# Optimization experiments

Measured on AMD Instinct MI355X. Metric: run time of the kernel, lower is better.

The kernel has to match this reference:

```python
import jax, jax.numpy as jnp
import numpy as np

N = 100000
B = 1024
NODE_DIM = 128
LATENT = 128
IN_DIM = NODE_DIM + 2 * LATENT   # 384, q/kv projection input width
FFN_IN = LATENT + IN_DIM          # 512, ffn input width


def setup_inputs() -> dict:
    key = jax.random.key(0)
    ks = jax.random.split(key, 16)
    s = 1.0 / np.sqrt(IN_DIM)
    s2 = 1.0 / np.sqrt(FFN_IN)
    s3 = 1.0 / np.sqrt(LATENT)
    return {
        "x": jax.random.normal(ks[0], (N, NODE_DIM), jnp.float32),
        "memory": jax.random.normal(ks[1], (N, LATENT), jnp.float32),
        "delta_t_vec": jax.random.normal(ks[2], (N, LATENT), jnp.float32),
        "tar_t_vec": jax.random.normal(ks[3], (B, LATENT), jnp.float32),
        # sparse neighbor mask, ~50 neighbors per target on average
        "neighbor_mask": jax.random.uniform(ks[4], (B, N)) < 5e-4,
        "tar_idx": jax.random.randint(ks[5], (B, 1), 0, N, jnp.int32),
        "Wq": jax.random.uniform(ks[6], (LATENT, IN_DIM), jnp.float32, -s, s),
        "bq": jnp.zeros((LATENT,), jnp.float32),
        "Wk": jax.random.uniform(ks[7], (LATENT, IN_DIM), jnp.float32, -s, s),
        "bk": jnp.zeros((LATENT,), jnp.float32),
        "Wv": jax.random.uniform(ks[8], (LATENT, IN_DIM), jnp.float32, -s, s),
        "bv": jnp.zeros((LATENT,), jnp.float32),
        "W1": jax.random.uniform(ks[9], (LATENT, FFN_IN), jnp.float32, -s2, s2),
        "b1": jnp.zeros((LATENT,), jnp.float32),
        "W2": jax.random.uniform(ks[10], (LATENT, LATENT), jnp.float32, -s3, s3),
        "b2": jnp.zeros((LATENT,), jnp.float32),
    }


def reference(x, memory, delta_t_vec, tar_t_vec, neighbor_mask, tar_idx,
              Wq, bq, Wk, bk, Wv, bv, W1, b1, W2, b2):
    idx = tar_idx[:, 0]                                  # [B]
    q_input = jnp.concatenate([x[idx], memory[idx], tar_t_vec], axis=-1)   # [B, IN_DIM]
    kv_input = jnp.concatenate([x, memory, delta_t_vec], axis=-1)          # [N, IN_DIM]
    q = q_input @ Wq.T + bq                              # [B, D]
    k = kv_input @ Wk.T + bk                             # [N, D]
    v = kv_input @ Wv.T + bv                             # [N, D]
    d = q.shape[-1]
    scores = jnp.einsum("bd,nd->bn", q, k) / jnp.sqrt(jnp.float32(d))      # [B, N]
    # rows with no neighbors attend to their own target node
    no_neighbor = ~jnp.any(neighbor_mask, axis=1)        # [B]
    self_mask = jnp.arange(neighbor_mask.shape[1])[None, :] == tar_idx     # [B, N]
    mask = neighbor_mask | (no_neighbor[:, None] & self_mask)
    scores = jnp.where(mask, scores, -jnp.inf)
    attn = jax.nn.softmax(scores, axis=-1)               # [B, N]
    agg = attn @ v                                       # [B, D]
    z = jnp.concatenate([agg, q_input], axis=-1)         # [B, FFN_IN]
    z = jax.nn.relu(z @ W1.T + b1) @ W2.T + b2           # [B, D]
    return z
```

## Files before the change

### kernel.cpp

```cpp
#include <hip/hip_runtime.h>
#include <stdint.h>
#include <stddef.h>

constexpr int N_NODES = 100000;
constexpr int BATCH   = 1024;
constexpr int LAT     = 128;
constexpr int INDIM   = 384;
constexpr int FFNIN   = 512;
constexpr int NB_MAX  = 512;

__global__ __launch_bounds__(384) void fused_graph_attn_kernel(
    const float* __restrict__ x,   const float* __restrict__ mem,
    const float* __restrict__ dtv, const float* __restrict__ ttv,
    const uint32_t* __restrict__ mask, const int* __restrict__ tar_idx,
    const float* __restrict__ Wq, const float* __restrict__ bq,
    const float* __restrict__ Wk, const float* __restrict__ bk,
    const float* __restrict__ Wv, const float* __restrict__ bv,
    const float* __restrict__ W1, const float* __restrict__ b1,
    const float* __restrict__ W2, const float* __restrict__ b2,
    float* __restrict__ out)
{
    const int b    = blockIdx.x;
    const int tid  = threadIdx.x;
    const int lane = tid & 63;
    const int wave = tid >> 6;

    __shared__ int   cnt;
    __shared__ int   jl[NB_MAX];
    __shared__ float sc[NB_MAX];
    __shared__ float qin[INDIM];
    __shared__ float qv[LAT];
    __shared__ float qk[INDIM];
    __shared__ float u[INDIM];
    __shared__ float zbuf[FFNIN];
    __shared__ float hbuf[LAT];
    __shared__ float sbias_sh;

    const int idx = tar_idx[b];
    if (tid == 0) cnt = 0;

    if (tid < 128)      qin[tid] = x[(size_t)idx * LAT + tid];
    else if (tid < 256) qin[tid] = mem[(size_t)idx * LAT + (tid - 128)];
    else                qin[tid] = ttv[(size_t)b * LAT + (tid - 256)];
    __syncthreads();

    {
        const uint4* row = (const uint4*)(mask + (size_t)b * N_NODES);
        for (int i = tid; i < N_NODES / 4; i += 384) {
            uint4 v = row[i];
            if (v.x | v.y | v.z | v.w) {
                uint32_t w[4] = {v.x, v.y, v.z, v.w};
                #pragma unroll
                for (int wi = 0; wi < 4; ++wi) {
                    if (w[wi]) {
                        int slot = atomicAdd(&cnt, 1);
                        if (slot < NB_MAX) jl[slot] = i * 4 + wi;
                    }
                }
            }
        }
    }
    __syncthreads();
    if (tid == 0 && cnt == 0) { jl[0] = idx; cnt = 1; }
    __syncthreads();
    const int nb = cnt < NB_MAX ? cnt : NB_MAX;

    if (tid < LAT) {
        const float4* wr = (const float4*)(Wq + (size_t)tid * INDIM);
        float acc = bq[tid];
        #pragma unroll 4
        for (int i = 0; i < INDIM / 4; ++i) {
            float4 w = wr[i];
            acc += w.x * qin[4*i] + w.y * qin[4*i+1] + w.z * qin[4*i+2] + w.w * qin[4*i+3];
        }
        qv[tid] = acc;
    }
    __syncthreads();

    {
        float acc = 0.f;
        #pragma unroll 8
        for (int d = 0; d < LAT; ++d) acc += qv[d] * Wk[(size_t)d * INDIM + tid];
        qk[tid] = acc;
    }
    if (wave == 0) {
        float p = qv[lane] * bk[lane] + qv[lane + 64] * bk[lane + 64];
        for (int off = 32; off; off >>= 1) p += __shfl_down(p, off, 64);
        if (lane == 0) sbias_sh = p;
    }
    __syncthreads();

    const float scale = 0.088388347648318447f;
    const float sb = sbias_sh;
    for (int jj = wave; jj < nb; jj += 6) {
        int j = jl[jj];
        const float* xp = x   + (size_t)j * LAT;
        const float* mp = mem + (size_t)j * LAT;
        const float* dp = dtv + (size_t)j * LAT;
        float p = qk[lane]       * xp[lane] + qk[lane + 64]  * xp[lane + 64]
                + qk[128 + lane] * mp[lane] + qk[192 + lane] * mp[lane + 64]
                + qk[256 + lane] * dp[lane] + qk[320 + lane] * dp[lane + 64];
        for (int off = 32; off; off >>= 1) p += __shfl_down(p, off, 64);
        if (lane == 0) sc[jj] = (p + sb) * scale;
    }
    __syncthreads();

    if (wave == 0) {
        float m = -INFINITY;
        for (int t = lane; t < nb; t += 64) m = fmaxf(m, sc[t]);
        for (int off = 32; off; off >>= 1) m = fmaxf(m, __shfl_down(m, off, 64));
        m = __shfl(m, 0, 64);
        float s = 0.f;
        for (int t = lane; t < nb; t += 64) { float e = __expf(sc[t] - m); sc[t] = e; s += e; }
        for (int off = 32; off; off >>= 1) s += __shfl_down(s, off, 64);
        s = __shfl(s, 0, 64);
        float inv = 1.f / s;
        for (int t = lane; t < nb; t += 64) sc[t] *= inv;
    }
    __syncthreads();

    {
        const float* src = (tid < 128) ? x : (tid < 256 ? mem : dtv);
        const int off128 = tid & 127;
        float acc = 0.f;
        for (int jj = 0; jj < nb; ++jj)
            acc += sc[jj] * src[(size_t)jl[jj] * LAT + off128];
        u[tid] = acc;
    }
    __syncthreads();

    if (tid < LAT) {
        const float4* wr = (const float4*)(Wv + (size_t)tid * INDIM);
        float acc = bv[tid];
        #pragma unroll 4
        for (int i = 0; i < INDIM / 4; ++i) {
            float4 w = wr[i];
            acc += w.x * u[4*i] + w.y * u[4*i+1] + w.z * u[4*i+2] + w.w * u[4*i+3];
        }
        zbuf[tid] = acc;
    }
    zbuf[LAT + tid] = qin[tid];
    __syncthreads();

    if (tid < LAT) {
        const float4* wr = (const float4*)(W1 + (size_t)tid * FFNIN);
        float acc = b1[tid];
        #pragma unroll 4
        for (int i = 0; i < FFNIN / 4; ++i) {
            float4 w = wr[i];
            acc += w.x * zbuf[4*i] + w.y * zbuf[4*i+1] + w.z * zbuf[4*i+2] + w.w * zbuf[4*i+3];
        }
        hbuf[tid] = fmaxf(acc, 0.f);
    }
    __syncthreads();

    if (tid < LAT) {
        const float4* wr = (const float4*)(W2 + (size_t)tid * LAT);
        float acc = b2[tid];
        #pragma unroll 4
        for (int i = 0; i < LAT / 4; ++i) {
            float4 w = wr[i];
            acc += w.x * hbuf[4*i] + w.y * hbuf[4*i+1] + w.z * hbuf[4*i+2] + w.w * hbuf[4*i+3];
        }
        out[(size_t)b * LAT + tid] = acc;
    }
}

extern "C" void kernel_launch(void* const* d_in, const int* in_sizes, int n_in,
                              void* d_out, int out_size, void* d_ws, size_t ws_size,
                              hipStream_t stream) {
    const float*    x    = (const float*)d_in[0];
    const float*    mem  = (const float*)d_in[1];
    const float*    dtv  = (const float*)d_in[2];
    const float*    ttv  = (const float*)d_in[3];
    const uint32_t* mask = (const uint32_t*)d_in[4];
    const int*      tidx = (const int*)d_in[5];
    const float*    Wq   = (const float*)d_in[6];
    const float*    bq   = (const float*)d_in[7];
    const float*    Wk   = (const float*)d_in[8];
    const float*    bk   = (const float*)d_in[9];
    const float*    Wv   = (const float*)d_in[10];
    const float*    bv   = (const float*)d_in[11];
    const float*    W1   = (const float*)d_in[12];
    const float*    b1   = (const float*)d_in[13];
    const float*    W2   = (const float*)d_in[14];
    const float*    b2   = (const float*)d_in[15];
    float* out = (float*)d_out;

    fused_graph_attn_kernel<<<BATCH, 384, 0, stream>>>(
        x, mem, dtv, ttv, mask, tidx, Wq, bq, Wk, bk, Wv, bv, W1, b1, W2, b2,
        out);
}
```

Before: 713.8 us.

## Overlap q projection with mask scan, fuse online softmax into aggregation

Wave 0 computes the q projection, the bias term and the qk = q·Wk vector while the other five waves scan the mask row using nontemporal loads. The score, softmax and weighted-sum phases are fused into one per-wave online-softmax pass, which removes the second gather of neighbor rows and two barriers. The per-wave partials are merged through shared memory. The final Wv, W1 and W2 matvecs are split across all 384 threads in three K-slices with a shared reduction. The catch is that only five waves scan the mask, and wave 0 does the serialized q/qk work alone.

```diff
diff --git a/kernel.cpp b/kernel.cpp
--- a/kernel.cpp
+++ b/kernel.cpp
@@ -8,6 +8,12 @@
 constexpr int INDIM   = 384;
 constexpr int FFNIN   = 512;
 constexpr int NB_MAX  = 512;
+
+typedef unsigned int u32x4 __attribute__((ext_vector_type(4)));
+
+__device__ __forceinline__ float dot4(float4 a, float4 b) {
+    return a.x * b.x + a.y * b.y + a.z * b.z + a.w * b.w;
+}
 
 __global__ __launch_bounds__(384) void fused_graph_attn_kernel(
     const float* __restrict__ x,   const float* __restrict__ mem,
@@ -25,16 +31,15 @@
     const int lane = tid & 63;
     const int wave = tid >> 6;
 
-    __shared__ int   cnt;
-    __shared__ int   jl[NB_MAX];
-    __shared__ float sc[NB_MAX];
-    __shared__ float qin[INDIM];
-    __shared__ float qv[LAT];
-    __shared__ float qk[INDIM];
-    __shared__ float u[INDIM];
-    __shared__ float zbuf[FFNIN];
-    __shared__ float hbuf[LAT];
-    __shared__ float sbias_sh;
+    __shared__ int cnt;
+    __shared__ int jl[NB_MAX];
+    __shared__ __align__(16) float qin[INDIM];
+    __shared__ __align__(16) float qk[INDIM];
+    __shared__ __align__(16) float u[INDIM];
+    __shared__ __align__(16) float zbuf[FFNIN];
+    __shared__ __align__(16) float hbuf[LAT];
+    __shared__ __align__(16) float upart[6][INDIM];
+    __shared__ float wm[6], ws[6], sbias_sh;
 
     const int idx = tar_idx[b];
     if (tid == 0) cnt = 0;
@@ -44,10 +49,41 @@
     else                qin[tid] = ttv[(size_t)b * LAT + (tid - 256)];
     __syncthreads();
 
-    {
-        const uint4* row = (const uint4*)(mask + (size_t)b * N_NODES);
-        for (int i = tid; i < N_NODES / 4; i += 384) {
-            uint4 v = row[i];
+    if (wave == 0) {
+        const float4* qin4 = (const float4*)qin;
+        const float4* r0 = (const float4*)(Wq + (size_t)lane * INDIM);
+        const float4* r1 = (const float4*)(Wq + (size_t)(lane + 64) * INDIM);
+        float a0 = bq[lane], a1 = bq[lane + 64];
+        #pragma unroll 4
+        for (int i = 0; i < INDIM / 4; ++i) {
+            float4 qi = qin4[i];
+            a0 += dot4(r0[i], qi);
+            a1 += dot4(r1[i], qi);
+        }
+        float sb = a0 * bk[lane] + a1 * bk[lane + 64];
+        #pragma unroll
+        for (int off = 1; off < 64; off <<= 1) sb += __shfl_xor(sb, off, 64);
+        if (lane == 0) sbias_sh = sb;
+        float qt[6] = {0.f, 0.f, 0.f, 0.f, 0.f, 0.f};
+        for (int l = 0; l < 64; ++l) {
+            float qd = __shfl(a0, l, 64);
+            const float* wkp = Wk + (size_t)l * INDIM + lane;
+            #pragma unroll
+            for (int t = 0; t < 6; ++t) qt[t] += qd * wkp[64 * t];
+        }
+        for (int l = 0; l < 64; ++l) {
+            float qd = __shfl(a1, l, 64);
+            const float* wkp = Wk + (size_t)(l + 64) * INDIM + lane;
+            #pragma unroll
+            for (int t = 0; t < 6; ++t) qt[t] += qd * wkp[64 * t];
+        }
+        #pragma unroll
+        for (int t = 0; t < 6; ++t) qk[lane + 64 * t] = qt[t];
+    } else {
+        const u32x4* row = (const u32x4*)(mask + (size_t)b * N_NODES);
+        #pragma unroll 2
+        for (int i = tid - 64; i < N_NODES / 4; i += 320) {
+            u32x4 v = __builtin_nontemporal_load(row + i);
             if (v.x | v.y | v.z | v.w) {
                 uint32_t w[4] = {v.x, v.y, v.z, v.w};
                 #pragma unroll
@@ -65,105 +101,102 @@
     __syncthreads();
     const int nb = cnt < NB_MAX ? cnt : NB_MAX;
 
-    if (tid < LAT) {
-        const float4* wr = (const float4*)(Wq + (size_t)tid * INDIM);
-        float acc = bq[tid];
-        #pragma unroll 4
-        for (int i = 0; i < INDIM / 4; ++i) {
-            float4 w = wr[i];
-            acc += w.x * qin[4*i] + w.y * qin[4*i+1] + w.z * qin[4*i+2] + w.w * qin[4*i+3];
-        }
-        qv[tid] = acc;
-    }
-    __syncthreads();
-
-    {
-        float acc = 0.f;
-        #pragma unroll 8
-        for (int d = 0; d < LAT; ++d) acc += qv[d] * Wk[(size_t)d * INDIM + tid];
-        qk[tid] = acc;
-    }
-    if (wave == 0) {
-        float p = qv[lane] * bk[lane] + qv[lane + 64] * bk[lane + 64];
-        for (int off = 32; off; off >>= 1) p += __shfl_down(p, off, 64);
-        if (lane == 0) sbias_sh = p;
-    }
-    __syncthreads();
-
     const float scale = 0.088388347648318447f;
     const float sb = sbias_sh;
+    float qkr[6];
+    #pragma unroll
+    for (int k = 0; k < 6; ++k) qkr[k] = qk[lane + 64 * k];
+
+    float m = -INFINITY, ssum = 0.f;
+    float ua[6] = {0.f, 0.f, 0.f, 0.f, 0.f, 0.f};
     for (int jj = wave; jj < nb; jj += 6) {
-        int j = jl[jj];
+        const int j = jl[jj];
         const float* xp = x   + (size_t)j * LAT;
         const float* mp = mem + (size_t)j * LAT;
         const float* dp = dtv + (size_t)j * LAT;
-        float p = qk[lane]       * xp[lane] + qk[lane + 64]  * xp[lane + 64]
-                + qk[128 + lane] * mp[lane] + qk[192 + lane] * mp[lane + 64]
-                + qk[256 + lane] * dp[lane] + qk[320 + lane] * dp[lane + 64];
-        for (int off = 32; off; off >>= 1) p += __shfl_down(p, off, 64);
-        if (lane == 0) sc[jj] = (p + sb) * scale;
-    }
-    __syncthreads();
-
-    if (wave == 0) {
-        float m = -INFINITY;
-        for (int t = lane; t < nb; t += 64) m = fmaxf(m, sc[t]);
-        for (int off = 32; off; off >>= 1) m = fmaxf(m, __shfl_down(m, off, 64));
-        m = __shfl(m, 0, 64);
-        float s = 0.f;
-        for (int t = lane; t < nb; t += 64) { float e = __expf(sc[t] - m); sc[t] = e; s += e; }
-        for (int off = 32; off; off >>= 1) s += __shfl_down(s, off, 64);
-        s = __shfl(s, 0, 64);
-        float inv = 1.f / s;
-        for (int t = lane; t < nb; t += 64) sc[t] *= inv;
-    }
-    __syncthreads();
-
-    {
-        const float* src = (tid < 128) ? x : (tid < 256 ? mem : dtv);
-        const int off128 = tid & 127;
+        const float f0 = xp[lane], f1 = xp[lane + 64];
+        const float f2 = mp[lane], f3 = mp[lane + 64];
+        const float f4 = dp[lane], f5 = dp[lane + 64];
+        float p = qkr[0] * f0 + qkr[1] * f1 + qkr[2] * f2
+                + qkr[3] * f3 + qkr[4] * f4 + qkr[5] * f5;
+        #pragma unroll
+        for (int off = 1; off < 64; off <<= 1) p += __shfl_xor(p, off, 64);
+        const float s    = (p + sb) * scale;
+        const float mn   = fmaxf(m, s);
+        const float corr = __expf(m - mn);
+        const float e    = __expf(s - mn);
+        ssum = ssum * corr + e;
+        ua[0] = ua[0] * corr + e * f0;  ua[1] = ua[1] * corr + e * f1;
+        ua[2] = ua[2] * corr + e * f2;  ua[3] = ua[3] * corr + e * f3;
+        ua[4] = ua[4] * corr + e * f4;  ua[5] = ua[5] * corr + e * f5;
+        m = mn;
+    }
+    if (lane == 0) { wm[wave] = m; ws[wave] = ssum; }
+    #pragma unroll
+    for (int k = 0; k < 6; ++k) upart[wave][lane + 64 * k] = ua[k];
+    __syncthreads();
+
+    {
+        float mstar = wm[0];
+        #pragma unroll
+        for (int w = 1; w < 6; ++w) mstar = fmaxf(mstar, wm[w]);
+        float num = 0.f, den = 0.f;
+        #pragma unroll
+        for (int w = 0; w < 6; ++w) {
+            const float c = __expf(wm[w] - mstar);
+            num += c * upart[w][tid];
+            den += c * ws[w];
+        }
+        u[tid] = num / den;
+    }
+    __syncthreads();
+
+    float* part = &upart[0][0];
+    const int o  = tid & 127;
+    const int pp = tid >> 7;
+
+    {
+        const float4* wr = (const float4*)(Wv + (size_t)o * INDIM);
+        const float4* uv = (const float4*)u;
+        const int i0 = pp * 32;
         float acc = 0.f;
-        for (int jj = 0; jj < nb; ++jj)
-            acc += sc[jj] * src[(size_t)jl[jj] * LAT + off128];
-        u[tid] = acc;
-    }
-    __syncthreads();
-
-    if (tid < LAT) {
-        const float4* wr = (const float4*)(Wv + (size_t)tid * INDIM);
-        float acc = bv[tid];
-        #pragma unroll 4
-        for (int i = 0; i < INDIM / 4; ++i) {
-            float4 w = wr[i];
-            acc += w.x * u[4*i] + w.y * u[4*i+1] + w.z * u[4*i+2] + w.w * u[4*i+3];
-        }
-        zbuf[tid] = acc;
+        #pragma unroll 4
+        for (int i = i0; i < i0 + 32; ++i) acc += dot4(wr[i], uv[i]);
+        part[pp * 128 + o] = acc;
     }
     zbuf[LAT + tid] = qin[tid];
     __syncthreads();
-
-    if (tid < LAT) {
-        const float4* wr = (const float4*)(W1 + (size_t)tid * FFNIN);
-        float acc = b1[tid];
-        #pragma unroll 4
-        for (int i = 0; i < FFNIN / 4; ++i) {
-            float4 w = wr[i];
-            acc += w.x * zbuf[4*i] + w.y * zbuf[4*i+1] + w.z * zbuf[4*i+2] + w.w * zbuf[4*i+3];
-        }
-        hbuf[tid] = fmaxf(acc, 0.f);
-    }
-    __syncthreads();
-
-    if (tid < LAT) {
-        const float4* wr = (const float4*)(W2 + (size_t)tid * LAT);
-        float acc = b2[tid];
-        #pragma unroll 4
-        for (int i = 0; i < LAT / 4; ++i) {
-            float4 w = wr[i];
-            acc += w.x * hbuf[4*i] + w.y * hbuf[4*i+1] + w.z * hbuf[4*i+2] + w.w * hbuf[4*i+3];
-        }
-        out[(size_t)b * LAT + tid] = acc;
-    }
+    if (tid < 128) zbuf[tid] = bv[tid] + part[tid] + part[128 + tid] + part[256 + tid];
+    __syncthreads();
+
+    {
+        const float4* wr = (const float4*)(W1 + (size_t)o * FFNIN);
+        const float4* zv = (const float4*)zbuf;
+        const int i0 = pp * 43;
+        const int i1 = (pp == 2) ? 128 : i0 + 43;
+        float acc = 0.f;
+        #pragma unroll 4
+        for (int i = i0; i < i1; ++i) acc += dot4(wr[i], zv[i]);
+        part[pp * 128 + o] = acc;
+    }
+    __syncthreads();
+    if (tid < 128)
+        hbuf[tid] = fmaxf(b1[tid] + part[tid] + part[128 + tid] + part[256 + tid], 0.f);
+    __syncthreads();
+
+    {
+        const float4* wr = (const float4*)(W2 + (size_t)o * LAT);
+        const float4* hv = (const float4*)hbuf;
+        const int i0 = pp * 11;
+        const int i1 = (pp == 2) ? 32 : i0 + 11;
+        float acc = 0.f;
+        #pragma unroll 4
+        for (int i = i0; i < i1; ++i) acc += dot4(wr[i], hv[i]);
+        part[pp * 128 + o] = acc;
+    }
+    __syncthreads();
+    if (tid < 128)
+        out[(size_t)b * LAT + tid] = b2[tid] + part[tid] + part[128 + tid] + part[256 + tid];
 }
 
 extern "C" void kernel_launch(void* const* d_in, const int* in_sizes, int n_in,
```

Measured after the change: 687.3 us. 3.7% less time.
